# Kernel tuning notes

Measured on AMD Instinct MI355X. Metric: run time of the kernel, lower is better.

## Reference

```python
import jax, jax.numpy as jnp
import numpy as np

SHORT = 2000
CUTVALS = [0, 2000, 12000, 40000, 100000]  # [0] + cutoffs + [n_classes]
OSZ = [10000, 28000, 60000]
HSZ = [384, 192, 96]
IN_F = 768
LN_EPS = 1e-5


def setup_inputs() -> dict:
    key = jax.random.key(0)
    ks = jax.random.split(key, 16)
    B, L = 256, 20
    inp = {
        "x": jax.random.normal(ks[0], (B, IN_F), jnp.float32),
        "head_W": jax.random.normal(ks[1], (SHORT + 3, IN_F), jnp.float32) / np.sqrt(IN_F),
        "target": jax.random.randint(ks[2], (B, L), 0, CUTVALS[-1], jnp.int64)
        if jax.config.jax_enable_x64 else jax.random.randint(ks[2], (B, L), 0, CUTVALS[-1], jnp.int32),
    }
    for i in range(3):
        inp[f"w1_{i}"] = jax.random.normal(ks[3 + 4 * i], (HSZ[i], IN_F), jnp.float32) / np.sqrt(IN_F)
        inp[f"g{i}"] = jnp.ones((HSZ[i],), jnp.float32)
        inp[f"b{i}"] = jnp.zeros((HSZ[i],), jnp.float32)
        inp[f"w2_{i}"] = jax.random.normal(ks[4 + 4 * i], (OSZ[i], HSZ[i]), jnp.float32) / np.sqrt(HSZ[i])
    return inp


def _bce_with_logits(logits, y):
    # matches torch BCEWithLogitsLoss(reduction='none')
    return jnp.maximum(logits, 0.0) - logits * y + jnp.log1p(jnp.exp(-jnp.abs(logits)))


def reference(x, head_W, w1_0, g0, b0, w2_0, w1_1, g1, b1, w2_1, w1_2, g2, b2, w2_2, target):
    W1, G, Bp, W2 = [w1_0, w1_1, w1_2], [g0, g1, g2], [b0, b1, b2], [w2_0, w2_1, w2_2]
    B = x.shape[0]
    rows = jnp.arange(B)[:, None]
    dt = x.dtype

    head_logits = x @ head_W.T  # [B, SHORT + n_clusters]

    # shortlist multi-hot (rows with no shortlist label stay all-zero, as in torch)
    m0 = target < SHORT
    onehot_short = jnp.zeros((B, SHORT), dt).at[rows, jnp.clip(target, 0, SHORT - 1)].max(m0.astype(dt))

    total_cluster = jnp.zeros((B,), dt)
    actives = []
    for i in range(3):
        low, high = CUTVALS[i + 1], CUTVALS[i + 2]
        osz = high - low
        m = (target >= low) & (target < high)  # [B, L]
        active = m.any(axis=1).astype(dt)      # [B]
        actives.append(active)
        # multi-hot targets for this cluster
        y = jnp.zeros((B, osz), dt).at[rows, jnp.clip(target - low, 0, osz - 1)].max(m.astype(dt))
        # tail projection: Linear -> LayerNorm -> ReLU -> Linear
        h = x @ W1[i].T
        mu = h.mean(-1, keepdims=True)
        var = ((h - mu) ** 2).mean(-1, keepdims=True)
        h = jax.nn.relu((h - mu) * jax.lax.rsqrt(var + LN_EPS) * G[i] + Bp[i])
        # p = sigmoid(cluster-root logit) * sigmoid(tail logits)
        root = jax.nn.sigmoid(head_logits[:, SHORT + i])[:, None]  # [B,1]
        p = root * jax.nn.sigmoid(h @ W2[i].T)                     # [B, osz]
        # torch BCELoss clamps log at -100
        bce = -(y * jnp.maximum(jnp.log(p), -100.0) + (1.0 - y) * jnp.maximum(jnp.log1p(-p), -100.0))
        total_cluster = total_cluster + active * bce.sum(axis=1)

    cluster_onehot = jnp.stack(actives, axis=1)  # [B, 3]
    head_y = jnp.concatenate([onehot_short, cluster_onehot], axis=1)
    head_loss = _bce_with_logits(head_logits, head_y)  # [B, SHORT+3]
    mult = (cluster_onehot == 0).astype(dt)
    head_loss = jnp.concatenate([head_loss[:, :SHORT], head_loss[:, SHORT:] * mult], axis=1)
    head_loss = head_loss.sum(axis=1)

    csz = jnp.asarray(OSZ, dt)
    num_loss = (mult + cluster_onehot * csz).sum(axis=1) + SHORT
    return ((head_loss + total_cluster) / num_loss).mean()
```

## Files before the change

### kernel.cpp

```cpp
#include <hip/hip_runtime.h>
#include <hip/hip_bf16.h>

#define INF 768
#define NSHORT 2000
#define NHEAD 2003

typedef __attribute__((ext_vector_type(8))) short  s16x8;
typedef __attribute__((ext_vector_type(4))) float  f32x4;
typedef __attribute__((ext_vector_type(8))) float  f32x8;

__device__ __forceinline__ float sigf(float z) { return 1.f / (1.f + __expf(-z)); }
__device__ __forceinline__ float softplusf(float z) {
    return fmaxf(z, 0.f) + __logf(1.f + __expf(-fabsf(z)));
}
__device__ __forceinline__ float qreduce16(float v) {
    v += __shfl_xor(v, 1); v += __shfl_xor(v, 2);
    v += __shfl_xor(v, 4); v += __shfl_xor(v, 8);
    return v;
}
__device__ __forceinline__ float wreduce64(float v) {
    v += __shfl_xor(v, 1);  v += __shfl_xor(v, 2);  v += __shfl_xor(v, 4);
    v += __shfl_xor(v, 8);  v += __shfl_xor(v, 16); v += __shfl_xor(v, 32);
    return v;
}
__device__ __forceinline__ short bfc(float x) {
    union { __hip_bfloat16 h; short s; } u; u.h = __float2bfloat16(x); return u.s;
}

template <int K32>
__device__ __forceinline__ void perm_B(const float* __restrict__ W, int N,
                                       __hip_bfloat16* __restrict__ dst, int c) {
    const int lane = c & 63, t2 = c >> 6;
    const int ct = t2 & 3, t3 = t2 >> 2;
    const int j = t3 % K32, stripe = t3 / K32;
    int col = stripe * 64 + ct * 16 + (lane & 15);
    if (col >= N) col = N - 1;
    const int k0 = j * 32 + (lane >> 4) * 8;
    const f32x8 v = *(const f32x8*)(W + (size_t)col * (K32 * 32) + k0);
    s16x8 o;
#pragma unroll
    for (int i = 0; i < 8; i++) o[i] = bfc(v[i]);
    *(s16x8*)((short*)dst + (size_t)c * 8) = o;
}
template <int K32>
__device__ __forceinline__ void perm_A(const float* __restrict__ X,
                                       __hip_bfloat16* __restrict__ dst, int c) {
    const int lane = c & 63, t2 = c >> 6;
    const int j = t2 % K32, rt = t2 / K32;
    const int row = rt * 16 + (lane & 15);
    const int k0 = j * 32 + (lane >> 4) * 8;
    const f32x8 v = *(const f32x8*)(X + (size_t)row * (K32 * 32) + k0);
    s16x8 o;
#pragma unroll
    for (int i = 0; i < 8; i++) o[i] = bfc(v[i]);
    *(s16x8*)((short*)dst + (size_t)c * 8) = o;
}

template <int K32, int RT, int MODE>
__device__ __forceinline__ void core_p(
    const __hip_bfloat16* __restrict__ Ap,
    const __hip_bfloat16* __restrict__ Wp, int N,
    int stripe, int rtb0,
    float* __restrict__ outH, int ldH,
    float* __restrict__ part, int pslot,
    const float* __restrict__ rootlogit, int ci)
{
    const int t = threadIdx.x;
    const int wave = t >> 6, lane = t & 63;
    const int quad = lane >> 4, l16 = lane & 15;
    const int rtb = rtb0 + wave * RT;

    const short* ap[RT];
#pragma unroll
    for (int rt = 0; rt < RT; rt++)
        ap[rt] = (const short*)Ap + ((size_t)(rtb + rt) * K32 * 64 + lane) * 8;
    const short* wp[4];
#pragma unroll
    for (int ct = 0; ct < 4; ct++)
        wp[ct] = (const short*)Wp + (((size_t)stripe * K32 * 4 + ct) * 64 + lane) * 8;

    s16x8 af[2][RT], wf[2][4];
#pragma unroll
    for (int rt = 0; rt < RT; rt++) af[0][rt] = *(const s16x8*)(ap[rt]);
#pragma unroll
    for (int ct = 0; ct < 4; ct++) wf[0][ct] = *(const s16x8*)(wp[ct]);

    f32x4 acc[RT][4];
#pragma unroll
    for (int rt = 0; rt < RT; rt++)
#pragma unroll
        for (int ct = 0; ct < 4; ct++) acc[rt][ct] = (f32x4){0.f, 0.f, 0.f, 0.f};

#pragma unroll
    for (int j = 0; j < K32; j++) {
        const int b = j & 1, nb = b ^ 1;
        if (j + 1 < K32) {
#pragma unroll
            for (int rt = 0; rt < RT; rt++)
                af[nb][rt] = *(const s16x8*)(ap[rt] + (size_t)(j + 1) * 512);
#pragma unroll
            for (int ct = 0; ct < 4; ct++)
                wf[nb][ct] = *(const s16x8*)(wp[ct] + (size_t)(j + 1) * 2048);
        }
#pragma unroll
        for (int rt = 0; rt < RT; rt++)
#pragma unroll
            for (int ct = 0; ct < 4; ct++)
                acc[rt][ct] = __builtin_amdgcn_mfma_f32_16x16x32_bf16(
                    af[b][rt], wf[b][ct], acc[rt][ct], 0, 0, 0);
    }

    const int col0 = stripe * 64;
    if (MODE == 0) {
#pragma unroll
        for (int rt = 0; rt < RT; rt++)
#pragma unroll
            for (int ct = 0; ct < 4; ct++) {
                const int col = col0 + ct * 16 + l16;
#pragma unroll
                for (int r = 0; r < 4; r++)
                    outH[(size_t)((rtb + rt) * 16 + quad * 4 + r) * ldH + col] = acc[rt][ct][r];
            }
    } else if (MODE == 1) {
#pragma unroll
        for (int rt = 0; rt < RT; rt++) {
#pragma unroll
            for (int r = 0; r < 4; r++) {
                const int row = (rtb + rt) * 16 + quad * 4 + r;
                float s = 0.f;
#pragma unroll
                for (int ct = 0; ct < 4; ct++) {
                    const int col = col0 + ct * 16 + l16;
                    if (col < NSHORT) s += softplusf(acc[rt][ct][r]);
                }
                s = qreduce16(s);
                if (l16 == 0) part[(size_t)row * 32 + pslot] = s;
            }
        }
    } else {
#pragma unroll
        for (int rt = 0; rt < RT; rt++) {
#pragma unroll
            for (int r = 0; r < 4; r++) {
                const int row = (rtb + rt) * 16 + quad * 4 + r;
                const float rv = sigf(rootlogit[row * 3 + ci]);
                float s = 0.f;
#pragma unroll
                for (int ct = 0; ct < 4; ct++) {
                    const int col = col0 + ct * 16 + l16;
                    if (col < N) {
                        const float p = rv * sigf(acc[rt][ct][r]);
                        s += -fmaxf(__logf(1.f - p), -100.f);
                    }
                }
                s = qreduce16(s);
                if (l16 == 0) part[(size_t)pslot * 256 + row] = s;
            }
        }
    }
}

__global__ __launch_bounds__(256) void k_pre(
    const float* __restrict__ x, const float* __restrict__ headW,
    const float* __restrict__ w10, const float* __restrict__ w11, const float* __restrict__ w12,
    const float* __restrict__ w20, const float* __restrict__ w21, const float* __restrict__ w22,
    __hip_bfloat16* xbp, __hip_bfloat16* hWp,
    __hip_bfloat16* w10p, __hip_bfloat16* w11p, __hip_bfloat16* w12p,
    __hip_bfloat16* w20p, __hip_bfloat16* w21p, __hip_bfloat16* w22p,
    float* __restrict__ rootlogit) {
    const int bx = blockIdx.x, t = threadIdx.x;
    if (bx < 256) {
        const int row = bx, wave = t >> 6, lane = t & 63;
        if (wave < 3) {
            const float* xr = x + row * INF;
            const float* wr = headW + (size_t)(NSHORT + wave) * INF;
            float s = 0.f;
            for (int k = lane; k < INF; k += 64) s += xr[k] * wr[k];
            s = wreduce64(s);
            if (lane == 0) rootlogit[row * 3 + wave] = s;
        }
    } else if (bx < 352)  perm_A<24>(x, xbp, (bx - 256) * 256 + t);
    else if (bx < 1120) perm_B<24>(headW, NHEAD, hWp, (bx - 352) * 256 + t);
    else if (bx < 1264) perm_B<24>(w10, 384, w10p, (bx - 1120) * 256 + t);
    else if (bx < 1336) perm_B<24>(w11, 192, w11p, (bx - 1264) * 256 + t);
    else if (bx < 1384) perm_B<24>(w12, 96, w12p, (bx - 1336) * 256 + t);
    else if (bx < 3268) perm_B<12>(w20, 10000, w20p, (bx - 1384) * 256 + t);
    else if (bx < 5896) perm_B<6>(w21, 28000, w21p, (bx - 3268) * 256 + t);
    else                perm_B<3>(w22, 60000, w22p, (bx - 5896) * 256 + t);
}

__global__ __launch_bounds__(256) void k_mm1(const __hip_bfloat16* __restrict__ xbp,
                                             const __hip_bfloat16* hWp,
                                             const __hip_bfloat16* w10p,
                                             const __hip_bfloat16* w11p,
                                             const __hip_bfloat16* w12p,
                                             float* __restrict__ phead,
                                             float* h0, float* h1, float* h2) {
    const int bx = blockIdx.x;
    if (bx < 64) {
        const int stripe = bx >> 1, rg = bx & 1;
        core_p<24, 2, 1>(xbp, hWp, NHEAD, stripe, rg * 8, nullptr, 0, phead, stripe, nullptr, 0);
    } else if (bx < 76) {
        const int m = bx - 64, stripe = m >> 1, rg = m & 1;
        core_p<24, 2, 0>(xbp, w10p, 384, stripe, rg * 8, h0, 384, nullptr, 0, nullptr, 0);
    } else if (bx < 82) {
        const int m = bx - 76, stripe = m >> 1, rg = m & 1;
        core_p<24, 2, 0>(xbp, w11p, 192, stripe, rg * 8, h1, 192, nullptr, 0, nullptr, 0);
    } else {
        const int m = bx - 82, stripe = m >> 1, rg = m & 1;
        core_p<24, 2, 0>(xbp, w12p, 96, stripe, rg * 8, h2, 96, nullptr, 0, nullptr, 0);
    }
}

__global__ __launch_bounds__(256) void k_ln(const float* h0, const float* h1, const float* h2,
                                            const float* g0, const float* g1, const float* g2,
                                            const float* b0, const float* b1, const float* b2,
                                            __hip_bfloat16* f0, __hip_bfloat16* f1,
                                            __hip_bfloat16* f2,
                                            __hip_bfloat16* p0, __hip_bfloat16* p1,
                                            __hip_bfloat16* p2) {
    const int task = blockIdx.x * 4 + (threadIdx.x >> 6);
    const int ci = task >> 8, row = task & 255, lane = threadIdx.x & 63;
    const float *h, *g, *bb; __hip_bfloat16 *fo, *po; int hsz, K32;
    if (ci == 0)      { h = h0; g = g0; bb = b0; fo = f0; po = p0; hsz = 384; K32 = 12; }
    else if (ci == 1) { h = h1; g = g1; bb = b1; fo = f1; po = p1; hsz = 192; K32 = 6; }
    else              { h = h2; g = g2; bb = b2; fo = f2; po = p2; hsz = 96;  K32 = 3; }
    const float* hr = h + row * hsz;
    float s = 0.f, s2 = 0.f;
    for (int k = lane; k < hsz; k += 64) { const float v = hr[k]; s += v; s2 += v * v; }
    s = wreduce64(s); s2 = wreduce64(s2);
    const float mu = s / hsz;
    const float var = s2 / hsz - mu * mu;
    const float rsn = rsqrtf(var + 1e-5f);
    const int nch = hsz >> 3;
    if (lane < nch) {
        const f32x8 v = *(const f32x8*)(hr + lane * 8);
        const f32x8 gg = *(const f32x8*)(g + lane * 8);
        const f32x8 bv = *(const f32x8*)(bb + lane * 8);
        s16x8 o;
#pragma unroll
        for (int i = 0; i < 8; i++)
            o[i] = bfc(fmaxf((v[i] - mu) * rsn * gg[i] + bv[i], 0.f));
        *(s16x8*)((short*)fo + (size_t)row * hsz + lane * 8) = o;
        const size_t chunk = ((size_t)(row >> 4) * K32 + (lane >> 2)) * 64 + (lane & 3) * 16 + (row & 15);
        *(s16x8*)((short*)po + chunk * 8) = o;
    }
}

__global__ __launch_bounds__(256, 2) void k_bce(const __hip_bfloat16* p0,
                                                const __hip_bfloat16* p1,
                                                const __hip_bfloat16* p2,
                                                const __hip_bfloat16* w20p,
                                                const __hip_bfloat16* w21p,
                                                const __hip_bfloat16* w22p,
                                                const __hip_bfloat16* f0,
                                                const __hip_bfloat16* f1,
                                                const __hip_bfloat16* f2,
                                                const float* w20, const float* w21, const float* w22,
                                                float* __restrict__ part,
                                                const float* __restrict__ rootlogit,
                                                const float* __restrict__ x,
                                                const float* __restrict__ headW,
                                                const int* __restrict__ target,
                                                float* __restrict__ corrbuf) {
    const int bx = blockIdx.x;
    if (bx >= 256) {
        const int gb = bx - 256;
        if (gb < 157)
            core_p<12, 4, 2>(p0, w20p, 10000, gb, 0, nullptr, 0, part, gb, rootlogit, 0);
        else if (gb < 595)
            core_p<6, 4, 2>(p1, w21p, 28000, gb - 157, 0, nullptr, 0, part, gb, rootlogit, 1);
        else
            core_p<3, 4, 2>(p2, w22p, 60000, gb - 595, 0, nullptr, 0, part, gb, rootlogit, 2);
    } else {
        const int row = bx;
        const int t = threadIdx.x, wave = t >> 6, lane = t & 63;
        __shared__ float sx[INF];
        __shared__ __hip_bfloat16 shb[384 + 192 + 96];
        __shared__ int st[20];
        __shared__ float scorr[4];
        for (int i = t; i < INF; i += 256) sx[i] = x[row * INF + i];
        for (int i = t; i < 384; i += 256) shb[i] = f0[row * 384 + i];
        for (int i = t; i < 192; i += 256) shb[384 + i] = f1[row * 192 + i];
        for (int i = t; i < 96; i += 256)  shb[576 + i] = f2[row * 96 + i];
        if (t < 20) st[t] = target[row * 20 + t];
        if (t < 4) scorr[t] = 0.f;
        __syncthreads();
        for (int l = wave; l < 20; l += 4) {
            const int tg = st[l];
            bool dup = false;
            for (int m = 0; m < l; m++) dup |= (st[m] == tg);
            if (dup) continue;
            if (tg < NSHORT) {
                const float* wr = headW + (size_t)tg * INF;
                float z = 0.f;
                for (int k = lane; k < INF; k += 64) z += sx[k] * wr[k];
                z = wreduce64(z);
                if (lane == 0) atomicAdd(&scorr[3], -z);
            } else {
                int ci, low, hsz, hoff; const float* w2;
                if (tg < 12000)      { ci = 0; low = 2000;  hsz = 384; hoff = 0;   w2 = w20; }
                else if (tg < 40000) { ci = 1; low = 12000; hsz = 192; hoff = 384; w2 = w21; }
                else                 { ci = 2; low = 40000; hsz = 96;  hoff = 576; w2 = w22; }
                const float* wr = w2 + (size_t)(tg - low) * hsz;
                float z = 0.f;
                for (int k = lane; k < hsz; k += 64)
                    z += __bfloat162float(shb[hoff + k]) * wr[k];
                z = wreduce64(z);
                if (lane == 0) {
                    const float rvv = sigf(rootlogit[row * 3 + ci]);
                    const float p = rvv * sigf(z);
                    atomicAdd(&scorr[ci],
                              -fmaxf(__logf(p), -100.f) + fmaxf(__logf(1.f - p), -100.f));
                }
            }
        }
        __syncthreads();
        if (t < 4) corrbuf[row * 4 + t] = scorr[t];
    }
}

__global__ __launch_bounds__(256) void k_red(const float* __restrict__ part,
                                             const float* __restrict__ phead,
                                             const float* __restrict__ corrbuf,
                                             const float* __restrict__ rootlogit,
                                             const int* __restrict__ target,
                                             float* __restrict__ out) {
    const int row = blockIdx.x, t = threadIdx.x;
    const int wave = t >> 6, lane = t & 63;
    float c0 = 0.f, c1 = 0.f, c2 = 0.f, hs = 0.f;
    for (int i = t; i < 1533; i += 256) {
        const float v = part[(size_t)i * 256 + row];
        if (i < 157) c0 += v; else if (i < 595) c1 += v; else c2 += v;
    }
    if (t < 32) hs = phead[row * 32 + t];
    c0 = wreduce64(c0); c1 = wreduce64(c1); c2 = wreduce64(c2); hs = wreduce64(hs);
    __shared__ float red[4][4];
    if (lane == 0) { red[0][wave] = c0; red[1][wave] = c1; red[2][wave] = c2; red[3][wave] = hs; }
    __syncthreads();
    if (t == 0) {
        float cc[3];
        for (int i = 0; i < 3; i++) cc[i] = red[i][0] + red[i][1] + red[i][2] + red[i][3];
        float hsum = red[3][0] + red[3][1] + red[3][2] + red[3][3] + corrbuf[row * 4 + 3];
        bool act[3] = {false, false, false};
        for (int l = 0; l < 20; l++) {
            const int tg = target[row * 20 + l];
            if (tg >= 2000) {
                if (tg < 12000) act[0] = true;
                else if (tg < 40000) act[1] = true;
                else act[2] = true;
            }
        }
        float total = 0.f, num = 2000.f;
        const float csz[3] = {10000.f, 28000.f, 60000.f};
        for (int i = 0; i < 3; i++) {
            if (act[i]) { total += cc[i] + corrbuf[row * 4 + i]; num += csz[i]; }
            else        { hsum += softplusf(rootlogit[row * 3 + i]); num += 1.f; }
        }
        atomicAdd(out, (hsum + total) / num * (1.f / 256.f));
    }
}

extern "C" void kernel_launch(void* const* d_in, const int* in_sizes, int n_in,
                              void* d_out, int out_size, void* d_ws, size_t ws_size,
                              hipStream_t stream) {
    const float* x      = (const float*)d_in[0];
    const float* headW  = (const float*)d_in[1];
    const int*   target = (const int*)d_in[2];
    const float* w10 = (const float*)d_in[3];
    const float* g0  = (const float*)d_in[4];
    const float* b0  = (const float*)d_in[5];
    const float* w20 = (const float*)d_in[6];
    const float* w11 = (const float*)d_in[7];
    const float* g1  = (const float*)d_in[8];
    const float* b1  = (const float*)d_in[9];
    const float* w21 = (const float*)d_in[10];
    const float* w12 = (const float*)d_in[11];
    const float* g2  = (const float*)d_in[12];
    const float* b2  = (const float*)d_in[13];
    const float* w22 = (const float*)d_in[14];
    float* out = (float*)d_out;

    char* ws = (char*)d_ws;
    size_t off = 0;
    auto carve = [&](size_t bytes) -> void* {
        void* p = ws + off;
        off += (bytes + 255) & ~(size_t)255;
        return p;
    };
    __hip_bfloat16* xbp  = (__hip_bfloat16*)carve((size_t)256 * 768 * 2);
    __hip_bfloat16* hWp  = (__hip_bfloat16*)carve((size_t)2048 * 768 * 2);
    __hip_bfloat16* w10p = (__hip_bfloat16*)carve((size_t)384 * 768 * 2);
    __hip_bfloat16* w11p = (__hip_bfloat16*)carve((size_t)192 * 768 * 2);
    __hip_bfloat16* w12p = (__hip_bfloat16*)carve((size_t)128 * 768 * 2);
    __hip_bfloat16* w20p = (__hip_bfloat16*)carve((size_t)10048 * 384 * 2);
    __hip_bfloat16* w21p = (__hip_bfloat16*)carve((size_t)28032 * 192 * 2);
    __hip_bfloat16* w22p = (__hip_bfloat16*)carve((size_t)60032 * 96 * 2);
    float* h0            = (float*)carve((size_t)256 * 384 * 4);
    float* h1            = (float*)carve((size_t)256 * 192 * 4);
    float* h2            = (float*)carve((size_t)256 * 96 * 4);
    __hip_bfloat16* f0   = (__hip_bfloat16*)carve((size_t)256 * 384 * 2);
    __hip_bfloat16* f1   = (__hip_bfloat16*)carve((size_t)256 * 192 * 2);
    __hip_bfloat16* f2   = (__hip_bfloat16*)carve((size_t)256 * 96 * 2);
    __hip_bfloat16* p0   = (__hip_bfloat16*)carve((size_t)256 * 384 * 2);
    __hip_bfloat16* p1   = (__hip_bfloat16*)carve((size_t)256 * 192 * 2);
    __hip_bfloat16* p2   = (__hip_bfloat16*)carve((size_t)256 * 96 * 2);
    float* rootlogit     = (float*)carve((size_t)256 * 3 * 4);
    float* phead         = (float*)carve((size_t)256 * 32 * 4);
    float* part          = (float*)carve((size_t)1536 * 256 * 4);
    float* corrbuf       = (float*)carve((size_t)256 * 4 * 4);

    hipMemsetAsync(out, 0, sizeof(float), stream);

    k_pre<<<8710, 256, 0, stream>>>(x, headW, w10, w11, w12, w20, w21, w22,
                                    xbp, hWp, w10p, w11p, w12p, w20p, w21p, w22p,
                                    rootlogit);
    k_mm1<<<86, 256, 0, stream>>>(xbp, hWp, w10p, w11p, w12p, phead, h0, h1, h2);
    k_ln<<<192, 256, 0, stream>>>(h0, h1, h2, g0, g1, g2, b0, b1, b2,
                                  f0, f1, f2, p0, p1, p2);
    k_bce<<<1789, 256, 0, stream>>>(p0, p1, p2, w20p, w21p, w22p, f0, f1, f2,
                                    w20, w21, w22, part, rootlogit, x, headW,
                                    target, corrbuf);
    k_red<<<256, 256, 0, stream>>>(part, phead, corrbuf, rootlogit, target, out);

    (void)in_sizes; (void)n_in; (void)out_size; (void)ws_size;
}
```

Baseline: 200.7 us.

## Split-K first GEMMs, halve BCE row tiles, move correction terms into reduction

```diff
diff --git a/kernel.cpp b/kernel.cpp
--- a/kernel.cpp
+++ b/kernel.cpp
@@ -60,7 +60,7 @@
 __device__ __forceinline__ void core_p(
     const __hip_bfloat16* __restrict__ Ap,
     const __hip_bfloat16* __restrict__ Wp, int N,
-    int stripe, int rtb0,
+    int stripe, int rtb0, int j0, int kstr,
     float* __restrict__ outH, int ldH,
     float* __restrict__ part, int pslot,
     const float* __restrict__ rootlogit, int ci)
@@ -73,11 +73,11 @@
     const short* ap[RT];
 #pragma unroll
     for (int rt = 0; rt < RT; rt++)
-        ap[rt] = (const short*)Ap + ((size_t)(rtb + rt) * K32 * 64 + lane) * 8;
+        ap[rt] = (const short*)Ap + (((size_t)(rtb + rt) * kstr + j0) * 64 + lane) * 8;
     const short* wp[4];
 #pragma unroll
     for (int ct = 0; ct < 4; ct++)
-        wp[ct] = (const short*)Wp + (((size_t)stripe * K32 * 4 + ct) * 64 + lane) * 8;
+        wp[ct] = (const short*)Wp + ((((size_t)stripe * kstr + j0) * 4 + ct) * 64 + lane) * 8;
 
     s16x8 af[2][RT], wf[2][4];
 #pragma unroll
@@ -117,26 +117,13 @@
 #pragma unroll
             for (int ct = 0; ct < 4; ct++) {
                 const int col = col0 + ct * 16 + l16;
-#pragma unroll
-                for (int r = 0; r < 4; r++)
-                    outH[(size_t)((rtb + rt) * 16 + quad * 4 + r) * ldH + col] = acc[rt][ct][r];
+                if (col < N) {
+#pragma unroll
+                    for (int r = 0; r < 4; r++)
+                        outH[(size_t)((rtb + rt) * 16 + quad * 4 + r) * ldH + col] =
+                            acc[rt][ct][r];
+                }
             }
-    } else if (MODE == 1) {
-#pragma unroll
-        for (int rt = 0; rt < RT; rt++) {
-#pragma unroll
-            for (int r = 0; r < 4; r++) {
-                const int row = (rtb + rt) * 16 + quad * 4 + r;
-                float s = 0.f;
-#pragma unroll
-                for (int ct = 0; ct < 4; ct++) {
-                    const int col = col0 + ct * 16 + l16;
-                    if (col < NSHORT) s += softplusf(acc[rt][ct][r]);
-                }
-                s = qreduce16(s);
-                if (l16 == 0) part[(size_t)row * 32 + pslot] = s;
-            }
-        }
     } else {
 #pragma unroll
         for (int rt = 0; rt < RT; rt++) {
@@ -144,15 +131,16 @@
             for (int r = 0; r < 4; r++) {
                 const int row = (rtb + rt) * 16 + quad * 4 + r;
                 const float rv = sigf(rootlogit[row * 3 + ci]);
-                float s = 0.f;
+                float pd = 1.f, pn = 1.f;
 #pragma unroll
                 for (int ct = 0; ct < 4; ct++) {
                     const int col = col0 + ct * 16 + l16;
-                    if (col < N) {
-                        const float p = rv * sigf(acc[rt][ct][r]);
-                        s += -fmaxf(__logf(1.f - p), -100.f);
-                    }
+                    const float tv = fminf(__expf(-acc[rt][ct][r]), 1e6f);
+                    const float d = (col < N) ? (1.f + tv) : 1.f;
+                    const float n = (col < N) ? (1.f + tv - rv) : 1.f;
+                    pd *= d; pn *= n;
                 }
+                float s = __logf(pd) - __logf(pn);
                 s = qreduce16(s);
                 if (l16 == 0) part[(size_t)pslot * 256 + row] = s;
             }
@@ -189,159 +177,190 @@
     else                perm_B<3>(w22, 60000, w22p, (bx - 5896) * 256 + t);
 }
 
-__global__ __launch_bounds__(256) void k_mm1(const __hip_bfloat16* __restrict__ xbp,
-                                             const __hip_bfloat16* hWp,
-                                             const __hip_bfloat16* w10p,
-                                             const __hip_bfloat16* w11p,
-                                             const __hip_bfloat16* w12p,
-                                             float* __restrict__ phead,
-                                             float* h0, float* h1, float* h2) {
+__global__ __launch_bounds__(256, 4) void k_mm1(const __hip_bfloat16* __restrict__ xbp,
+                                                const __hip_bfloat16* hWp,
+                                                const __hip_bfloat16* w10p,
+                                                const __hip_bfloat16* w11p,
+                                                const __hip_bfloat16* w12p,
+                                                float* zA, float* zB,
+                                                float* h0a, float* h0b,
+                                                float* h1a, float* h1b,
+                                                float* h2a, float* h2b) {
     const int bx = blockIdx.x;
-    if (bx < 64) {
-        const int stripe = bx >> 1, rg = bx & 1;
-        core_p<24, 2, 1>(xbp, hWp, NHEAD, stripe, rg * 8, nullptr, 0, phead, stripe, nullptr, 0);
-    } else if (bx < 76) {
-        const int m = bx - 64, stripe = m >> 1, rg = m & 1;
-        core_p<24, 2, 0>(xbp, w10p, 384, stripe, rg * 8, h0, 384, nullptr, 0, nullptr, 0);
-    } else if (bx < 82) {
-        const int m = bx - 76, stripe = m >> 1, rg = m & 1;
-        core_p<24, 2, 0>(xbp, w11p, 192, stripe, rg * 8, h1, 192, nullptr, 0, nullptr, 0);
+    if (bx < 128) {
+        const int kq = bx & 1, rg = (bx >> 1) & 1, stripe = bx >> 2;
+        core_p<12, 2, 0>(xbp, hWp, NHEAD, stripe, rg * 8, kq * 12, 24,
+                         kq ? zB : zA, 2048, nullptr, 0, nullptr, 0);
+    } else if (bx < 152) {
+        const int m = bx - 128, stripe = m >> 2, rg = (m >> 1) & 1, kq = m & 1;
+        core_p<12, 2, 0>(xbp, w10p, 384, stripe, rg * 8, kq * 12, 24,
+                         kq ? h0b : h0a, 384, nullptr, 0, nullptr, 0);
+    } else if (bx < 164) {
+        const int m = bx - 152, stripe = m >> 2, rg = (m >> 1) & 1, kq = m & 1;
+        core_p<12, 2, 0>(xbp, w11p, 192, stripe, rg * 8, kq * 12, 24,
+                         kq ? h1b : h1a, 192, nullptr, 0, nullptr, 0);
     } else {
-        const int m = bx - 82, stripe = m >> 1, rg = m & 1;
-        core_p<24, 2, 0>(xbp, w12p, 96, stripe, rg * 8, h2, 96, nullptr, 0, nullptr, 0);
-    }
-}
-
-__global__ __launch_bounds__(256) void k_ln(const float* h0, const float* h1, const float* h2,
+        const int m = bx - 164, stripe = m >> 2, rg = (m >> 1) & 1, kq = m & 1;
+        core_p<12, 2, 0>(xbp, w12p, 96, stripe, rg * 8, kq * 12, 24,
+                         kq ? h2b : h2a, 96, nullptr, 0, nullptr, 0);
+    }
+}
+
+__global__ __launch_bounds__(256) void k_ln(const float* h0a, const float* h0b,
+                                            const float* h1a, const float* h1b,
+                                            const float* h2a, const float* h2b,
                                             const float* g0, const float* g1, const float* g2,
                                             const float* b0, const float* b1, const float* b2,
+                                            const float* zA, const float* zB,
                                             __hip_bfloat16* f0, __hip_bfloat16* f1,
                                             __hip_bfloat16* f2,
                                             __hip_bfloat16* p0, __hip_bfloat16* p1,
-                                            __hip_bfloat16* p2) {
-    const int task = blockIdx.x * 4 + (threadIdx.x >> 6);
-    const int ci = task >> 8, row = task & 255, lane = threadIdx.x & 63;
-    const float *h, *g, *bb; __hip_bfloat16 *fo, *po; int hsz, K32;
-    if (ci == 0)      { h = h0; g = g0; bb = b0; fo = f0; po = p0; hsz = 384; K32 = 12; }
-    else if (ci == 1) { h = h1; g = g1; bb = b1; fo = f1; po = p1; hsz = 192; K32 = 6; }
-    else              { h = h2; g = g2; bb = b2; fo = f2; po = p2; hsz = 96;  K32 = 3; }
-    const float* hr = h + row * hsz;
-    float s = 0.f, s2 = 0.f;
-    for (int k = lane; k < hsz; k += 64) { const float v = hr[k]; s += v; s2 += v * v; }
-    s = wreduce64(s); s2 = wreduce64(s2);
-    const float mu = s / hsz;
-    const float var = s2 / hsz - mu * mu;
-    const float rsn = rsqrtf(var + 1e-5f);
-    const int nch = hsz >> 3;
-    if (lane < nch) {
-        const f32x8 v = *(const f32x8*)(hr + lane * 8);
-        const f32x8 gg = *(const f32x8*)(g + lane * 8);
-        const f32x8 bv = *(const f32x8*)(bb + lane * 8);
-        s16x8 o;
-#pragma unroll
-        for (int i = 0; i < 8; i++)
-            o[i] = bfc(fmaxf((v[i] - mu) * rsn * gg[i] + bv[i], 0.f));
-        *(s16x8*)((short*)fo + (size_t)row * hsz + lane * 8) = o;
-        const size_t chunk = ((size_t)(row >> 4) * K32 + (lane >> 2)) * 64 + (lane & 3) * 16 + (row & 15);
-        *(s16x8*)((short*)po + chunk * 8) = o;
-    }
-}
-
-__global__ __launch_bounds__(256, 2) void k_bce(const __hip_bfloat16* p0,
+                                            __hip_bfloat16* p2,
+                                            float* __restrict__ phead) {
+    const int bx = blockIdx.x;
+    if (bx < 192) {
+        const int task = bx * 4 + (threadIdx.x >> 6);
+        const int ci = task >> 8, row = task & 255, lane = threadIdx.x & 63;
+        const float *ha, *hb, *g, *bb; __hip_bfloat16 *fo, *po; int hsz, K32;
+        if (ci == 0)      { ha = h0a; hb = h0b; g = g0; bb = b0; fo = f0; po = p0; hsz = 384; K32 = 12; }
+        else if (ci == 1) { ha = h1a; hb = h1b; g = g1; bb = b1; fo = f1; po = p1; hsz = 192; K32 = 6; }
+        else              { ha = h2a; hb = h2b; g = g2; bb = b2; fo = f2; po = p2; hsz = 96;  K32 = 3; }
+        const float* hra = ha + row * hsz;
+        const float* hrb = hb + row * hsz;
+        float s = 0.f, s2 = 0.f;
+        for (int k = lane; k < hsz; k += 64) {
+            const float v = hra[k] + hrb[k]; s += v; s2 += v * v;
+        }
+        s = wreduce64(s); s2 = wreduce64(s2);
+        const float mu = s / hsz;
+        const float var = s2 / hsz - mu * mu;
+        const float rsn = rsqrtf(var + 1e-5f);
+        const int nch = hsz >> 3;
+        if (lane < nch) {
+            const f32x8 va = *(const f32x8*)(hra + lane * 8);
+            const f32x8 vb = *(const f32x8*)(hrb + lane * 8);
+            const f32x8 gg = *(const f32x8*)(g + lane * 8);
+            const f32x8 bv = *(const f32x8*)(bb + lane * 8);
+            s16x8 o;
+#pragma unroll
+            for (int i = 0; i < 8; i++)
+                o[i] = bfc(fmaxf((va[i] + vb[i] - mu) * rsn * gg[i] + bv[i], 0.f));
+            *(s16x8*)((short*)fo + (size_t)row * hsz + lane * 8) = o;
+            const size_t chunk = ((size_t)(row >> 4) * K32 + (lane >> 2)) * 64
+                               + (lane & 3) * 16 + (row & 15);
+            *(s16x8*)((short*)po + chunk * 8) = o;
+        }
+    } else {
+        const int row = bx - 192, t = threadIdx.x;
+        const int wave = t >> 6, lane = t & 63;
+        float val = 0.f;
+        if (t < 250) {
+            const f32x8 a = *(const f32x8*)(zA + (size_t)row * 2048 + t * 8);
+            const f32x8 b = *(const f32x8*)(zB + (size_t)row * 2048 + t * 8);
+            float m = 0.f, P = 1.f;
+#pragma unroll
+            for (int i = 0; i < 8; i++) {
+                const float z = a[i] + b[i];
+                m += fmaxf(z, 0.f);
+                P *= 1.f + __expf(-fabsf(z));
+            }
+            val = m + __logf(P);
+        }
+        val = wreduce64(val);
+        __shared__ float red[4];
+        if (lane == 0) red[wave] = val;
+        __syncthreads();
+        if (t == 0) phead[row] = red[0] + red[1] + red[2] + red[3];
+    }
+}
+
+__global__ __launch_bounds__(256, 4) void k_bce(const __hip_bfloat16* p0,
                                                 const __hip_bfloat16* p1,
                                                 const __hip_bfloat16* p2,
                                                 const __hip_bfloat16* w20p,
                                                 const __hip_bfloat16* w21p,
                                                 const __hip_bfloat16* w22p,
-                                                const __hip_bfloat16* f0,
-                                                const __hip_bfloat16* f1,
-                                                const __hip_bfloat16* f2,
-                                                const float* w20, const float* w21, const float* w22,
                                                 float* __restrict__ part,
-                                                const float* __restrict__ rootlogit,
-                                                const float* __restrict__ x,
-                                                const float* __restrict__ headW,
-                                                const int* __restrict__ target,
-                                                float* __restrict__ corrbuf) {
+                                                const float* __restrict__ rootlogit) {
     const int bx = blockIdx.x;
-    if (bx >= 256) {
-        const int gb = bx - 256;
-        if (gb < 157)
-            core_p<12, 4, 2>(p0, w20p, 10000, gb, 0, nullptr, 0, part, gb, rootlogit, 0);
-        else if (gb < 595)
-            core_p<6, 4, 2>(p1, w21p, 28000, gb - 157, 0, nullptr, 0, part, gb, rootlogit, 1);
-        else
-            core_p<3, 4, 2>(p2, w22p, 60000, gb - 595, 0, nullptr, 0, part, gb, rootlogit, 2);
-    } else {
-        const int row = bx;
-        const int t = threadIdx.x, wave = t >> 6, lane = t & 63;
-        __shared__ float sx[INF];
-        __shared__ __hip_bfloat16 shb[384 + 192 + 96];
-        __shared__ int st[20];
-        __shared__ float scorr[4];
-        for (int i = t; i < INF; i += 256) sx[i] = x[row * INF + i];
-        for (int i = t; i < 384; i += 256) shb[i] = f0[row * 384 + i];
-        for (int i = t; i < 192; i += 256) shb[384 + i] = f1[row * 192 + i];
-        for (int i = t; i < 96; i += 256)  shb[576 + i] = f2[row * 96 + i];
-        if (t < 20) st[t] = target[row * 20 + t];
-        if (t < 4) scorr[t] = 0.f;
-        __syncthreads();
-        for (int l = wave; l < 20; l += 4) {
-            const int tg = st[l];
-            bool dup = false;
-            for (int m = 0; m < l; m++) dup |= (st[m] == tg);
-            if (dup) continue;
-            if (tg < NSHORT) {
-                const float* wr = headW + (size_t)tg * INF;
-                float z = 0.f;
-                for (int k = lane; k < INF; k += 64) z += sx[k] * wr[k];
-                z = wreduce64(z);
-                if (lane == 0) atomicAdd(&scorr[3], -z);
-            } else {
-                int ci, low, hsz, hoff; const float* w2;
-                if (tg < 12000)      { ci = 0; low = 2000;  hsz = 384; hoff = 0;   w2 = w20; }
-                else if (tg < 40000) { ci = 1; low = 12000; hsz = 192; hoff = 384; w2 = w21; }
-                else                 { ci = 2; low = 40000; hsz = 96;  hoff = 576; w2 = w22; }
-                const float* wr = w2 + (size_t)(tg - low) * hsz;
-                float z = 0.f;
-                for (int k = lane; k < hsz; k += 64)
-                    z += __bfloat162float(shb[hoff + k]) * wr[k];
-                z = wreduce64(z);
-                if (lane == 0) {
-                    const float rvv = sigf(rootlogit[row * 3 + ci]);
-                    const float p = rvv * sigf(z);
-                    atomicAdd(&scorr[ci],
-                              -fmaxf(__logf(p), -100.f) + fmaxf(__logf(1.f - p), -100.f));
-                }
-            }
-        }
-        __syncthreads();
-        if (t < 4) corrbuf[row * 4 + t] = scorr[t];
-    }
+    const int s = bx >> 1, rg = bx & 1;
+    if (s < 157)
+        core_p<12, 2, 2>(p0, w20p, 10000, s, rg * 8, 0, 12,
+                         nullptr, 0, part, s, rootlogit, 0);
+    else if (s < 595)
+        core_p<6, 2, 2>(p1, w21p, 28000, s - 157, rg * 8, 0, 6,
+                        nullptr, 0, part, s, rootlogit, 1);
+    else
+        core_p<3, 2, 2>(p2, w22p, 60000, s - 595, rg * 8, 0, 3,
+                        nullptr, 0, part, s, rootlogit, 2);
 }
 
 __global__ __launch_bounds__(256) void k_red(const float* __restrict__ part,
                                              const float* __restrict__ phead,
-                                             const float* __restrict__ corrbuf,
                                              const float* __restrict__ rootlogit,
                                              const int* __restrict__ target,
+                                             const float* __restrict__ x,
+                                             const float* __restrict__ headW,
+                                             const __hip_bfloat16* f0,
+                                             const __hip_bfloat16* f1,
+                                             const __hip_bfloat16* f2,
+                                             const float* w20, const float* w21, const float* w22,
                                              float* __restrict__ out) {
-    const int row = blockIdx.x, t = threadIdx.x;
-    const int wave = t >> 6, lane = t & 63;
-    float c0 = 0.f, c1 = 0.f, c2 = 0.f, hs = 0.f;
+    const int row = blockIdx.x;
+    const int t = threadIdx.x, wave = t >> 6, lane = t & 63;
+    __shared__ float sx[INF];
+    __shared__ __hip_bfloat16 shb[384 + 192 + 96];
+    __shared__ int st[20];
+    __shared__ float scorr[4];
+    __shared__ float red[4][4];
+    for (int i = t; i < INF; i += 256) sx[i] = x[row * INF + i];
+    for (int i = t; i < 384; i += 256) shb[i] = f0[row * 384 + i];
+    for (int i = t; i < 192; i += 256) shb[384 + i] = f1[row * 192 + i];
+    for (int i = t; i < 96; i += 256)  shb[576 + i] = f2[row * 96 + i];
+    if (t < 20) st[t] = target[row * 20 + t];
+    if (t < 4) scorr[t] = 0.f;
+    __syncthreads();
+    for (int l = wave; l < 20; l += 4) {
+        const int tg = st[l];
+        bool dup = false;
+        for (int m = 0; m < l; m++) dup |= (st[m] == tg);
+        if (dup) continue;
+        if (tg < NSHORT) {
+            const float* wr = headW + (size_t)tg * INF;
+            float z = 0.f;
+            for (int k = lane; k < INF; k += 64) z += sx[k] * wr[k];
+            z = wreduce64(z);
+            if (lane == 0) atomicAdd(&scorr[3], -z);
+        } else {
+            int ci, low, hsz, hoff; const float* w2;
+            if (tg < 12000)      { ci = 0; low = 2000;  hsz = 384; hoff = 0;   w2 = w20; }
+            else if (tg < 40000) { ci = 1; low = 12000; hsz = 192; hoff = 384; w2 = w21; }
+            else                 { ci = 2; low = 40000; hsz = 96;  hoff = 576; w2 = w22; }
+            const float* wr = w2 + (size_t)(tg - low) * hsz;
+            float z = 0.f;
+            for (int k = lane; k < hsz; k += 64)
+                z += __bfloat162float(shb[hoff + k]) * wr[k];
+            z = wreduce64(z);
+            if (lane == 0) {
+                const float rvv = sigf(rootlogit[row * 3 + ci]);
+                const float p = rvv * sigf(z);
+                atomicAdd(&scorr[ci],
+                          -fmaxf(__logf(p), -100.f) + fmaxf(__logf(1.f - p), -100.f));
+            }
+        }
+    }
+    float c0 = 0.f, c1 = 0.f, c2 = 0.f;
     for (int i = t; i < 1533; i += 256) {
         const float v = part[(size_t)i * 256 + row];
         if (i < 157) c0 += v; else if (i < 595) c1 += v; else c2 += v;
     }
-    if (t < 32) hs = phead[row * 32 + t];
-    c0 = wreduce64(c0); c1 = wreduce64(c1); c2 = wreduce64(c2); hs = wreduce64(hs);
-    __shared__ float red[4][4];
-    if (lane == 0) { red[0][wave] = c0; red[1][wave] = c1; red[2][wave] = c2; red[3][wave] = hs; }
+    c0 = wreduce64(c0); c1 = wreduce64(c1); c2 = wreduce64(c2);
+    if (lane == 0) { red[0][wave] = c0; red[1][wave] = c1; red[2][wave] = c2; }
     __syncthreads();
     if (t == 0) {
         float cc[3];
         for (int i = 0; i < 3; i++) cc[i] = red[i][0] + red[i][1] + red[i][2] + red[i][3];
-        float hsum = red[3][0] + red[3][1] + red[3][2] + red[3][3] + corrbuf[row * 4 + 3];
+        float hsum = phead[row] + scorr[3];
         bool act[3] = {false, false, false};
         for (int l = 0; l < 20; l++) {
             const int tg = target[row * 20 + l];
@@ -354,7 +373,7 @@
         float total = 0.f, num = 2000.f;
         const float csz[3] = {10000.f, 28000.f, 60000.f};
         for (int i = 0; i < 3; i++) {
-            if (act[i]) { total += cc[i] + corrbuf[row * 4 + i]; num += csz[i]; }
+            if (act[i]) { total += cc[i] + scorr[i]; num += csz[i]; }
             else        { hsum += softplusf(rootlogit[row * 3 + i]); num += 1.f; }
         }
         atomicAdd(out, (hsum + total) / num * (1.f / 256.f));
@@ -396,9 +415,14 @@
     __hip_bfloat16* w20p = (__hip_bfloat16*)carve((size_t)10048 * 384 * 2);
     __hip_bfloat16* w21p = (__hip_bfloat16*)carve((size_t)28032 * 192 * 2);
     __hip_bfloat16* w22p = (__hip_bfloat16*)carve((size_t)60032 * 96 * 2);
-    float* h0            = (float*)carve((size_t)256 * 384 * 4);
-    float* h1            = (float*)carve((size_t)256 * 192 * 4);
-    float* h2            = (float*)carve((size_t)256 * 96 * 4);
+    float* zA            = (float*)carve((size_t)256 * 2048 * 4);
+    float* zB            = (float*)carve((size_t)256 * 2048 * 4);
+    float* h0a           = (float*)carve((size_t)256 * 384 * 4);
+    float* h0b           = (float*)carve((size_t)256 * 384 * 4);
+    float* h1a           = (float*)carve((size_t)256 * 192 * 4);
+    float* h1b           = (float*)carve((size_t)256 * 192 * 4);
+    float* h2a           = (float*)carve((size_t)256 * 96 * 4);
+    float* h2b           = (float*)carve((size_t)256 * 96 * 4);
     __hip_bfloat16* f0   = (__hip_bfloat16*)carve((size_t)256 * 384 * 2);
     __hip_bfloat16* f1   = (__hip_bfloat16*)carve((size_t)256 * 192 * 2);
     __hip_bfloat16* f2   = (__hip_bfloat16*)carve((size_t)256 * 96 * 2);
@@ -406,22 +430,22 @@
     __hip_bfloat16* p1   = (__hip_bfloat16*)carve((size_t)256 * 192 * 2);
     __hip_bfloat16* p2   = (__hip_bfloat16*)carve((size_t)256 * 96 * 2);
     float* rootlogit     = (float*)carve((size_t)256 * 3 * 4);
-    float* phead         = (float*)carve((size_t)256 * 32 * 4);
+    float* phead         = (float*)carve((size_t)256 * 4);
     float* part          = (float*)carve((size_t)1536 * 256 * 4);
-    float* corrbuf       = (float*)carve((size_t)256 * 4 * 4);
 
     hipMemsetAsync(out, 0, sizeof(float), stream);
 
     k_pre<<<8710, 256, 0, stream>>>(x, headW, w10, w11, w12, w20, w21, w22,
                                     xbp, hWp, w10p, w11p, w12p, w20p, w21p, w22p,
                                     rootlogit);
-    k_mm1<<<86, 256, 0, stream>>>(xbp, hWp, w10p, w11p, w12p, phead, h0, h1, h2);
-    k_ln<<<192, 256, 0, stream>>>(h0, h1, h2, g0, g1, g2, b0, b1, b2,
-                                  f0, f1, f2, p0, p1, p2);
-    k_bce<<<1789, 256, 0, stream>>>(p0, p1, p2, w20p, w21p, w22p, f0, f1, f2,
-                                    w20, w21, w22, part, rootlogit, x, headW,
-                                    target, corrbuf);
-    k_red<<<256, 256, 0, stream>>>(part, phead, corrbuf, rootlogit, target, out);
+    k_mm1<<<172, 256, 0, stream>>>(xbp, hWp, w10p, w11p, w12p,
+                                   zA, zB, h0a, h0b, h1a, h1b, h2a, h2b);
+    k_ln<<<448, 256, 0, stream>>>(h0a, h0b, h1a, h1b, h2a, h2b,
+                                  g0, g1, g2, b0, b1, b2, zA, zB,
+                                  f0, f1, f2, p0, p1, p2, phead);
+    k_bce<<<3066, 256, 0, stream>>>(p0, p1, p2, w20p, w21p, w22p, part, rootlogit);
+    k_red<<<256, 256, 0, stream>>>(part, phead, rootlogit, target, x, headW,
+                                   f0, f1, f2, w20, w21, w22, out);
 
     (void)in_sizes; (void)n_in; (void)out_size; (void)ws_size;
 }
```

New measurement: 186.1 us. 7.3% less time.
